# Performance work log

Measured on AMD Instinct MI355X. Metric: run time of the kernel, lower is better.

## Reference

```python
import jax, jax.numpy as jnp
import numpy as np

N_HEADS = 16
D_MODEL = 1024
HEAD_D = D_MODEL // N_HEADS


def setup_inputs() -> dict:
    key = jax.random.key(0)
    ks = jax.random.split(key, 8)
    B, S, D = 4, 2048, D_MODEL
    scale = 1.0 / np.sqrt(D)
    return {
        "query": jax.random.normal(ks[0], (B, S, D), jnp.float32),
        "key": jax.random.normal(ks[1], (B, S, D), jnp.float32),
        "value": jax.random.normal(ks[2], (B, S, D), jnp.float32),
        "mask": jax.random.randint(ks[3], (B, S, S), 0, 2, jnp.int32),
        "wq": jax.random.normal(ks[4], (D, D), jnp.float32) * scale,
        "wk": jax.random.normal(ks[5], (D, D), jnp.float32) * scale,
        "wv": jax.random.normal(ks[6], (D, D), jnp.float32) * scale,
        "w_out": jax.random.normal(ks[7], (D, D), jnp.float32) * scale,
    }


def reference(query, key, value, mask, wq, wk, wv, w_out):
    B, Sq, D = query.shape
    H, hd = N_HEADS, HEAD_D

    def split(x):  # (B,S,D) -> (B,H,S,hd)
        return x.reshape(B, -1, H, hd).transpose(0, 2, 1, 3)

    # torch Linear: y = x @ W.T (weights here stored as [out,in])
    Q = split(jnp.einsum('bsd,ed->bse', query, wq))
    K = split(jnp.einsum('bsd,ed->bse', key, wk))
    V = split(jnp.einsum('bsd,ed->bse', value, wv))

    scores = jnp.einsum('bhqd,bhkd->bhqk', Q, K) / np.sqrt(hd)
    scores = jnp.where(mask[:, None, :, :] == 1, jnp.float32(-1e9), scores)
    attn = jax.nn.softmax(scores, axis=-1)
    out = jnp.einsum('bhqk,bhkd->bhqd', attn, V)
    out = out.transpose(0, 2, 1, 3).reshape(B, Sq, D)
    return jnp.einsum('bsd,ed->bse', out, w_out)
```

## Files before the change

kernel.cpp:

```cpp
#include <hip/hip_runtime.h>
#include <hip/hip_bf16.h>


typedef __attribute__((ext_vector_type(8))) short short8;
typedef __attribute__((ext_vector_type(4))) float f32x4;
typedef __attribute__((ext_vector_type(4))) unsigned int u32x4;
typedef unsigned short u16;
typedef unsigned int u32;
typedef unsigned long long u64;

#define GLD16(gp, lp) __builtin_amdgcn_global_load_lds( \
    (const __attribute__((address_space(1))) void*)(gp), \
    (__attribute__((address_space(3))) void*)(lp), 16, 0, 0)

#if __has_builtin(__builtin_amdgcn_exp2f)
#define EXP2F(x) __builtin_amdgcn_exp2f(x)
#else
#define EXP2F(x) exp2f(x)
#endif

__device__ __forceinline__ u16 f2bf(float f) {
  u32 u = __builtin_bit_cast(u32, f);
  return (u16)((u + 0x7FFFu + ((u >> 16) & 1u)) >> 16);
}
__device__ __forceinline__ u32 swz64(u32 b)  { return b ^ (((b >> 7) & 3u) << 4); }
__device__ __forceinline__ u32 swz128(u32 b) { return b ^ (((b >> 7) & 7u) << 4); }

__global__ __launch_bounds__(256) void cvt_kernel(const float* __restrict__ in,
                                                  u16* __restrict__ out, float scale) {
  const size_t i = (size_t)blockIdx.x * 256 + threadIdx.x;
  f32x4 a = *(const f32x4*)(in + i * 8);
  f32x4 b = *(const f32x4*)(in + i * 8 + 4);
  u32x4 w;
  w.x = (u32)f2bf(a[0] * scale) | ((u32)f2bf(a[1] * scale) << 16);
  w.y = (u32)f2bf(a[2] * scale) | ((u32)f2bf(a[3] * scale) << 16);
  w.z = (u32)f2bf(b[0] * scale) | ((u32)f2bf(b[1] * scale) << 16);
  w.w = (u32)f2bf(b[2] * scale) | ((u32)f2bf(b[3] * scale) << 16);
  *(u32x4*)(out + i * 8) = w;
}

__global__ __launch_bounds__(256) void pack_mask_kernel(const int* __restrict__ m,
                                                        u64* __restrict__ out) {
  const size_t i = (size_t)blockIdx.x * 256 + threadIdx.x;
  u64 bal = __ballot(m[i] == 1);
  if ((threadIdx.x & 63) == 0) out[i >> 6] = bal;
}

template <int MODE>
__global__ __launch_bounds__(256)
void gemm_bt(const u16* __restrict__ A, const u16* __restrict__ W,
             void* __restrict__ outp, int K_) {
  __shared__ alignas(16) char sm[16384];
  const int tid = threadIdx.x, lane = tid & 63, wid = tid >> 6;
  const int g = lane >> 4, ln16 = lane & 15;
  const int wr = wid >> 1, wc = wid & 1;
  const int bm = blockIdx.y * 128, bn = blockIdx.x * 128;
  const int ldb = K_ * 2;

  u32 aoff[4], boff[4];
#pragma unroll
  for (int t = 0; t < 4; ++t) {
    aoff[t] = swz64(((u32)(wr * 64 + t * 16 + ln16) << 6) + ((u32)g << 4));
    boff[t] = 8192u + swz64(((u32)(wc * 64 + t * 16 + ln16) << 6) + ((u32)g << 4));
  }
  const char* ga[2]; const char* gw[2]; u32 doff[2];
#pragma unroll
  for (int i = 0; i < 2; ++i) {
    u32 lb = swz64((u32)(tid + i * 256) << 4);
    u32 row = lb >> 6, kbyte = lb & 63;
    ga[i] = (const char*)A + (size_t)(bm + row) * ldb + kbyte;
    gw[i] = (const char*)W + (size_t)(bn + row) * ldb + kbyte;
    doff[i] = (u32)(wid * 1024 + i * 4096);
  }
  f32x4 acc[4][4] = {};
  const int nk = K_ >> 5;
  for (int kt = 0; kt < nk; ++kt) {
    __syncthreads();
#pragma unroll
    for (int i = 0; i < 2; ++i) {
      GLD16(ga[i], sm + doff[i]);
      GLD16(gw[i], sm + 8192 + doff[i]);
      ga[i] += 64; gw[i] += 64;
    }
    __syncthreads();
    short8 aF[4], bF[4];
#pragma unroll
    for (int t = 0; t < 4; ++t) aF[t] = *(const short8*)(sm + aoff[t]);
#pragma unroll
    for (int t = 0; t < 4; ++t) bF[t] = *(const short8*)(sm + boff[t]);
#pragma unroll
    for (int mt = 0; mt < 4; ++mt)
#pragma unroll
      for (int nt = 0; nt < 4; ++nt)
        acc[mt][nt] = __builtin_amdgcn_mfma_f32_16x16x32_bf16(aF[mt], bF[nt], acc[mt][nt], 0, 0, 0);
  }
#pragma unroll
  for (int mt = 0; mt < 4; ++mt)
#pragma unroll
    for (int nt = 0; nt < 4; ++nt) {
      const f32x4 v = acc[mt][nt];
      const int row0 = bm + wr * 64 + mt * 16 + g * 4;
      const int col = bn + wc * 64 + nt * 16 + ln16;
      if (MODE == 2) {
        float* o = (float*)outp;
#pragma unroll
        for (int r = 0; r < 4; ++r) o[(size_t)(row0 + r) * 1024 + col] = v[r];
      } else if (MODE == 0) {
        u16* o = (u16*)outp;
        const int h = col >> 6, d = col & 63;
#pragma unroll
        for (int r = 0; r < 4; ++r) {
          const int row = row0 + r, b = row >> 11, s = row & 2047;
          o[((size_t)(b * 16 + h) * 2048 + s) * 64 + d] = f2bf(v[r]);
        }
      } else {
        u16* o = (u16*)outp;
        const int h = col >> 6, d = col & 63;
        const int b = row0 >> 11, s = row0 & 2047;
        u64 pv = (u64)f2bf(v[0]) | ((u64)f2bf(v[1]) << 16) |
                 ((u64)f2bf(v[2]) << 32) | ((u64)f2bf(v[3]) << 48);
        *(u64*)&o[((size_t)(b * 16 + h) * 64 + d) * 2048 + s] = pv;
      }
    }
}

__global__ __launch_bounds__(256)
void attn_kernel(const u16* __restrict__ Qh, const u16* __restrict__ Kh,
                 const u16* __restrict__ Vt, const u64* __restrict__ mp,
                 u16* __restrict__ AO) {
  __shared__ alignas(16) char sm[32768];
  const int tid = threadIdx.x, lane = tid & 63, wid = tid >> 6;
  const int g = lane >> 4, ln16 = lane & 15;
  char* Pl = sm + 16384 + wid * 4096;
  const int h = blockIdx.y, b = blockIdx.z;
  const int bh = b * 16 + h;
  const int q0 = blockIdx.x * 128 + wid * 32;
  const u16* Qb = Qh + (size_t)bh * 2048 * 64;
  const char* Kb = (const char*)Kh + (size_t)bh * 2048 * 128;
  const char* Vb = (const char*)Vt + (size_t)bh * 64 * 4096;

  short8 qf[2][2];
#pragma unroll
  for (int qs = 0; qs < 2; ++qs)
#pragma unroll
    for (int s = 0; s < 2; ++s)
      qf[qs][s] = *(const short8*)(Qb + (size_t)(q0 + qs * 16 + ln16) * 64 + s * 32 + g * 8);

  f32x4 acc[2][4] = {};
  float mx[2] = {-1e30f, -1e30f};
  float ls[2] = {0.f, 0.f};

  u32 srow[2], sbyt[2];
#pragma unroll
  for (int i = 0; i < 2; ++i) {
    u32 lb = swz128((u32)(tid + i * 256) << 4);
    srow[i] = lb >> 7; sbyt[i] = lb & 127;
  }
  const u64* mq = mp + ((size_t)b * 2048 + q0 + ln16) * 32;

  for (int kv = 0; kv < 2048; kv += 64) {
    __syncthreads();
#pragma unroll
    for (int i = 0; i < 2; ++i) {
      const u32 doff = (u32)(wid * 1024 + i * 4096);
      GLD16(Kb + (size_t)(kv + srow[i]) * 128 + sbyt[i], sm + doff);
      GLD16(Vb + (size_t)srow[i] * 4096 + (size_t)kv * 2 + sbyt[i], sm + 8192 + doff);
    }
    __syncthreads();

    u64 mw0 = mq[kv >> 6];
    u64 mw1 = mq[512 + (kv >> 6)];

    f32x4 sc[2][4] = {};
#pragma unroll
    for (int s = 0; s < 2; ++s)
#pragma unroll
      for (int kt = 0; kt < 4; ++kt) {
        short8 kf = *(const short8*)(sm + swz128(((u32)(kt * 16 + ln16) << 7) + s * 64 + g * 16));
        sc[0][kt] = __builtin_amdgcn_mfma_f32_16x16x32_bf16(kf, qf[0][s], sc[0][kt], 0, 0, 0);
        sc[1][kt] = __builtin_amdgcn_mfma_f32_16x16x32_bf16(kf, qf[1][s], sc[1][kt], 0, 0, 0);
      }

#pragma unroll
    for (int qs = 0; qs < 2; ++qs) {
      const u64 mw = qs ? mw1 : mw0;
      float tm = sc[qs][0][0];
#pragma unroll
      for (int kt = 0; kt < 4; ++kt)
#pragma unroll
        for (int r = 0; r < 4; ++r) tm = fmaxf(tm, sc[qs][kt][r]);
      tm = fmaxf(tm, __shfl_xor(tm, 16, 64));
      tm = fmaxf(tm, __shfl_xor(tm, 32, 64));
      const float mn = fmaxf(mx[qs], tm);
      const float corr = EXP2F(mx[qs] - mn);
      mx[qs] = mn;
      const u32 lo = (u32)mw, hi = (u32)(mw >> 32);
      float ps = 0.f;
#pragma unroll
      for (int kt = 0; kt < 4; ++kt) {
        const u32 nib = (((kt < 2) ? lo : hi) >> ((kt & 1) * 16 + g * 4)) & 0xFu;
        u64 pv = 0;
#pragma unroll
        for (int r = 0; r < 4; ++r) {
          float p = EXP2F(sc[qs][kt][r] - mn);
          if (nib & (1u << r)) p = 0.f;
          ps += p;
          pv |= (u64)f2bf(p) << (16 * r);
        }
        *(u64*)(Pl + swz128(((u32)(qs * 16 + ln16) << 7) + (u32)(kt * 32 + g * 8))) = pv;
      }
      ps += __shfl_xor(ps, 16, 64);
      ps += __shfl_xor(ps, 32, 64);
      ls[qs] = ls[qs] * corr + ps;
#pragma unroll
      for (int dt = 0; dt < 4; ++dt) acc[qs][dt] = acc[qs][dt] * corr;
    }
    asm volatile("" ::: "memory");

#pragma unroll
    for (int s = 0; s < 2; ++s) {
      short8 pf0 = *(const short8*)(Pl + swz128(((u32)ln16 << 7) + s * 64 + g * 16));
      short8 pf1 = *(const short8*)(Pl + swz128(((u32)(16 + ln16) << 7) + s * 64 + g * 16));
#pragma unroll
      for (int dt = 0; dt < 4; ++dt) {
        short8 vf = *(const short8*)(sm + 8192 + swz128(((u32)(dt * 16 + ln16) << 7) + s * 64 + g * 16));
        acc[0][dt] = __builtin_amdgcn_mfma_f32_16x16x32_bf16(vf, pf0, acc[0][dt], 0, 0, 0);
        acc[1][dt] = __builtin_amdgcn_mfma_f32_16x16x32_bf16(vf, pf1, acc[1][dt], 0, 0, 0);
      }
    }
    asm volatile("" ::: "memory");
  }

#pragma unroll
  for (int qs = 0; qs < 2; ++qs) {
    const float rl = 1.0f / ls[qs];
    const int q = q0 + qs * 16 + ln16;
#pragma unroll
    for (int dt = 0; dt < 4; ++dt) {
      const f32x4 v = acc[qs][dt];
      u64 pv = (u64)f2bf(v[0] * rl) | ((u64)f2bf(v[1] * rl) << 16) |
               ((u64)f2bf(v[2] * rl) << 32) | ((u64)f2bf(v[3] * rl) << 48);
      *(u64*)(AO + ((size_t)b * 2048 + q) * 1024 + h * 64 + dt * 16 + g * 4) = pv;
    }
  }
}

extern "C" void kernel_launch(void* const* d_in, const int* in_sizes, int n_in,
                              void* d_out, int out_size, void* d_ws, size_t ws_size,
                              hipStream_t stream) {
  const float* q   = (const float*)d_in[0];
  const float* k   = (const float*)d_in[1];
  const float* v   = (const float*)d_in[2];
  const int*   msk = (const int*)d_in[3];
  const float* wq  = (const float*)d_in[4];
  const float* wk  = (const float*)d_in[5];
  const float* wv  = (const float*)d_in[6];
  const float* wo  = (const float*)d_in[7];

  char* ws = (char*)d_ws;
  const size_t SZX = (size_t)8192 * 1024 * 2;
  const size_t SZW = (size_t)1024 * 1024 * 2;
  u16* qb  = (u16*)(ws + 0 * SZX);
  u16* kb  = (u16*)(ws + 1 * SZX);
  u16* vb  = (u16*)(ws + 2 * SZX);
  u16* wqb = (u16*)(ws + 3 * SZX + 0 * SZW);
  u16* wkb = (u16*)(ws + 3 * SZX + 1 * SZW);
  u16* wvb = (u16*)(ws + 3 * SZX + 2 * SZW);
  u16* wob = (u16*)(ws + 3 * SZX + 3 * SZW);
  u16* Qh  = (u16*)(ws + 3 * SZX + 4 * SZW);
  u16* Kh  = (u16*)(ws + 4 * SZX + 4 * SZW);
  u16* Vtp = (u16*)(ws + 5 * SZX + 4 * SZW);
  u16* AO  = qb;
  u64* mp  = (u64*)(ws + 6 * SZX + 4 * SZW);

  const float QSCALE = 0.18033688011112042f;

  cvt_kernel<<<4096, 256, 0, stream>>>(q, qb, 1.0f);
  cvt_kernel<<<4096, 256, 0, stream>>>(k, kb, 1.0f);
  cvt_kernel<<<4096, 256, 0, stream>>>(v, vb, 1.0f);
  cvt_kernel<<<512, 256, 0, stream>>>(wq, wqb, QSCALE);
  cvt_kernel<<<512, 256, 0, stream>>>(wk, wkb, 1.0f);
  cvt_kernel<<<512, 256, 0, stream>>>(wv, wvb, 1.0f);
  cvt_kernel<<<512, 256, 0, stream>>>(wo, wob, 1.0f);
  pack_mask_kernel<<<65536, 256, 0, stream>>>(msk, mp);

  gemm_bt<0><<<dim3(8, 64), 256, 0, stream>>>(qb, wqb, (void*)Qh, 1024);
  gemm_bt<0><<<dim3(8, 64), 256, 0, stream>>>(kb, wkb, (void*)Kh, 1024);
  gemm_bt<1><<<dim3(8, 64), 256, 0, stream>>>(vb, wvb, (void*)Vtp, 1024);

  attn_kernel<<<dim3(16, 16, 4), 256, 0, stream>>>(Qh, Kh, Vtp, mp, AO);

  gemm_bt<2><<<dim3(8, 64), 256, 0, stream>>>(AO, wob, d_out, 1024);
}
```

Baseline: 527.8 us.

## Double-buffer GEMM and attention loads, keep P in registers, use hardware bf16 convert

The GEMM now uses a 64-wide K tile with two LDS buffers, so the next tile's global-to-LDS load is issued before the current tile is computed. The attention kernel double-buffers K/V tiles the same way and prefetches mask words. It also keeps softmax probabilities in registers and feeds them to 16x16x16 MFMAs, which removes the LDS round trip for P. Manual bf16 rounding is replaced by v_cvt_pk_bf16_f32 throughout. The double buffering still has only one barrier per iteration, which could race between the async load into one buffer and reads of the previous one. The larger LDS use (64KB per GEMM block) may also reduce occupancy.

```diff
diff --git a/kernel.cpp b/kernel.cpp
--- a/kernel.cpp
+++ b/kernel.cpp
@@ -3,7 +3,9 @@
 
 
 typedef __attribute__((ext_vector_type(8))) short short8;
+typedef __attribute__((ext_vector_type(4))) short s16x4;
 typedef __attribute__((ext_vector_type(4))) float f32x4;
+typedef __attribute__((ext_vector_type(2))) unsigned int u32x2;
 typedef __attribute__((ext_vector_type(4))) unsigned int u32x4;
 typedef unsigned short u16;
 typedef unsigned int u32;
@@ -19,11 +21,30 @@
 #define EXP2F(x) exp2f(x)
 #endif
 
+#define MFMA32(a, b, c) __builtin_amdgcn_mfma_f32_16x16x32_bf16(a, b, c, 0, 0, 0)
+
+#if __has_builtin(__builtin_amdgcn_mfma_f32_16x16x16bf16_1k)
+__device__ __forceinline__ f32x4 mfma16(s16x4 a, s16x4 b, f32x4 c) {
+  return __builtin_amdgcn_mfma_f32_16x16x16bf16_1k(a, b, c, 0, 0, 0);
+}
+#else
+__device__ __forceinline__ f32x4 mfma16(s16x4 a, s16x4 b, f32x4 c) {
+  f32x4 d;
+  asm("v_mfma_f32_16x16x16_bf16 %0, %1, %2, %3"
+      : "=v"(d) : "v"(a), "v"(b), "0"(c));
+  return d;
+}
+#endif
+
 __device__ __forceinline__ u16 f2bf(float f) {
   u32 u = __builtin_bit_cast(u32, f);
   return (u16)((u + 0x7FFFu + ((u >> 16) & 1u)) >> 16);
 }
-__device__ __forceinline__ u32 swz64(u32 b)  { return b ^ (((b >> 7) & 3u) << 4); }
+__device__ __forceinline__ u32 cvtpk(float lo, float hi) {
+  u32 r;
+  asm("v_cvt_pk_bf16_f32 %0, %1, %2" : "=v"(r) : "v"(lo), "v"(hi));
+  return r;
+}
 __device__ __forceinline__ u32 swz128(u32 b) { return b ^ (((b >> 7) & 7u) << 4); }
 
 __global__ __launch_bounds__(256) void cvt_kernel(const float* __restrict__ in,
@@ -32,10 +53,10 @@
   f32x4 a = *(const f32x4*)(in + i * 8);
   f32x4 b = *(const f32x4*)(in + i * 8 + 4);
   u32x4 w;
-  w.x = (u32)f2bf(a[0] * scale) | ((u32)f2bf(a[1] * scale) << 16);
-  w.y = (u32)f2bf(a[2] * scale) | ((u32)f2bf(a[3] * scale) << 16);
-  w.z = (u32)f2bf(b[0] * scale) | ((u32)f2bf(b[1] * scale) << 16);
-  w.w = (u32)f2bf(b[2] * scale) | ((u32)f2bf(b[3] * scale) << 16);
+  w.x = cvtpk(a[0] * scale, a[1] * scale);
+  w.y = cvtpk(a[2] * scale, a[3] * scale);
+  w.z = cvtpk(b[0] * scale, b[1] * scale);
+  w.w = cvtpk(b[2] * scale, b[3] * scale);
   *(u32x4*)(out + i * 8) = w;
 }
 
@@ -50,49 +71,61 @@
 __global__ __launch_bounds__(256)
 void gemm_bt(const u16* __restrict__ A, const u16* __restrict__ W,
              void* __restrict__ outp, int K_) {
-  __shared__ alignas(16) char sm[16384];
+  __shared__ alignas(16) char sm[65536];
   const int tid = threadIdx.x, lane = tid & 63, wid = tid >> 6;
   const int g = lane >> 4, ln16 = lane & 15;
   const int wr = wid >> 1, wc = wid & 1;
   const int bm = blockIdx.y * 128, bn = blockIdx.x * 128;
   const int ldb = K_ * 2;
 
-  u32 aoff[4], boff[4];
-#pragma unroll
-  for (int t = 0; t < 4; ++t) {
-    aoff[t] = swz64(((u32)(wr * 64 + t * 16 + ln16) << 6) + ((u32)g << 4));
-    boff[t] = 8192u + swz64(((u32)(wc * 64 + t * 16 + ln16) << 6) + ((u32)g << 4));
-  }
-  const char* ga[2]; const char* gw[2]; u32 doff[2];
-#pragma unroll
-  for (int i = 0; i < 2; ++i) {
-    u32 lb = swz64((u32)(tid + i * 256) << 4);
-    u32 row = lb >> 6, kbyte = lb & 63;
+  u32 abase[2], bbase[2];
+#pragma unroll
+  for (int kk = 0; kk < 2; ++kk) {
+    const u32 sb = ((u32)(kk * 64 + g * 16)) ^ (((u32)ln16 & 7u) << 4);
+    abase[kk] = ((u32)(wr * 64 + ln16) << 7) + sb;
+    bbase[kk] = 16384u + ((u32)(wc * 64 + ln16) << 7) + sb;
+  }
+  const char* ga[4]; const char* gw[4];
+#pragma unroll
+  for (int i = 0; i < 4; ++i) {
+    u32 lb = swz128((u32)(tid + i * 256) << 4);
+    u32 row = lb >> 7, kbyte = lb & 127;
     ga[i] = (const char*)A + (size_t)(bm + row) * ldb + kbyte;
     gw[i] = (const char*)W + (size_t)(bn + row) * ldb + kbyte;
-    doff[i] = (u32)(wid * 1024 + i * 4096);
   }
   f32x4 acc[4][4] = {};
-  const int nk = K_ >> 5;
+  const int nk = K_ >> 6;
+  int cur = 0;
+
+#define G_STAGE(BUF)                                                  \
+  {                                                                   \
+    char* dst = sm + (BUF) * 32768 + wid * 1024;                      \
+    _Pragma("unroll") for (int i = 0; i < 4; ++i) {                   \
+      GLD16(ga[i], dst + i * 4096);                                   \
+      GLD16(gw[i], dst + 16384 + i * 4096);                           \
+      ga[i] += 128; gw[i] += 128;                                     \
+    }                                                                 \
+  }
+
+  G_STAGE(0);
   for (int kt = 0; kt < nk; ++kt) {
     __syncthreads();
-#pragma unroll
-    for (int i = 0; i < 2; ++i) {
-      GLD16(ga[i], sm + doff[i]);
-      GLD16(gw[i], sm + 8192 + doff[i]);
-      ga[i] += 64; gw[i] += 64;
-    }
-    __syncthreads();
-    short8 aF[4], bF[4];
-#pragma unroll
-    for (int t = 0; t < 4; ++t) aF[t] = *(const short8*)(sm + aoff[t]);
-#pragma unroll
-    for (int t = 0; t < 4; ++t) bF[t] = *(const short8*)(sm + boff[t]);
-#pragma unroll
-    for (int mt = 0; mt < 4; ++mt)
-#pragma unroll
-      for (int nt = 0; nt < 4; ++nt)
-        acc[mt][nt] = __builtin_amdgcn_mfma_f32_16x16x32_bf16(aF[mt], bF[nt], acc[mt][nt], 0, 0, 0);
+    if (kt + 1 < nk) G_STAGE(cur ^ 1);
+    const char* cb = sm + cur * 32768;
+#pragma unroll
+    for (int kk = 0; kk < 2; ++kk) {
+      short8 aF[4], bF[4];
+#pragma unroll
+      for (int t = 0; t < 4; ++t) aF[t] = *(const short8*)(cb + abase[kk] + t * 2048);
+#pragma unroll
+      for (int t = 0; t < 4; ++t) bF[t] = *(const short8*)(cb + bbase[kk] + t * 2048);
+#pragma unroll
+      for (int mt = 0; mt < 4; ++mt)
+#pragma unroll
+        for (int nt = 0; nt < 4; ++nt)
+          acc[mt][nt] = MFMA32(aF[mt], bF[nt], acc[mt][nt]);
+    }
+    cur ^= 1;
   }
 #pragma unroll
   for (int mt = 0; mt < 4; ++mt)
@@ -117,11 +150,11 @@
         u16* o = (u16*)outp;
         const int h = col >> 6, d = col & 63;
         const int b = row0 >> 11, s = row0 & 2047;
-        u64 pv = (u64)f2bf(v[0]) | ((u64)f2bf(v[1]) << 16) |
-                 ((u64)f2bf(v[2]) << 32) | ((u64)f2bf(v[3]) << 48);
-        *(u64*)&o[((size_t)(b * 16 + h) * 64 + d) * 2048 + s] = pv;
+        u32x2 pv; pv.x = cvtpk(v[0], v[1]); pv.y = cvtpk(v[2], v[3]);
+        *(u32x2*)&o[((size_t)(b * 16 + h) * 64 + d) * 2048 + s] = pv;
       }
     }
+#undef G_STAGE
 }
 
 __global__ __launch_bounds__(256)
@@ -131,9 +164,7 @@
   __shared__ alignas(16) char sm[32768];
   const int tid = threadIdx.x, lane = tid & 63, wid = tid >> 6;
   const int g = lane >> 4, ln16 = lane & 15;
-  char* Pl = sm + 16384 + wid * 4096;
-  const int h = blockIdx.y, b = blockIdx.z;
-  const int bh = b * 16 + h;
+  const int h = blockIdx.y, b = blockIdx.z, bh = b * 16 + h;
   const int q0 = blockIdx.x * 128 + wid * 32;
   const u16* Qb = Qh + (size_t)bh * 2048 * 64;
   const char* Kb = (const char*)Kh + (size_t)bh * 2048 * 128;
@@ -156,31 +187,49 @@
     u32 lb = swz128((u32)(tid + i * 256) << 4);
     srow[i] = lb >> 7; sbyt[i] = lb & 127;
   }
+  u32 kbase[2];
+#pragma unroll
+  for (int s = 0; s < 2; ++s)
+    kbase[s] = ((u32)ln16 << 7) + (((u32)(s * 64 + g * 16)) ^ (((u32)ln16 & 7u) << 4));
+  u32 vbyt[4];
+#pragma unroll
+  for (int kt = 0; kt < 4; ++kt)
+    vbyt[kt] = 8192u + ((u32)ln16 << 7) + (((u32)(kt * 32 + g * 8)) ^ (((u32)ln16 & 7u) << 4));
+
   const u64* mq = mp + ((size_t)b * 2048 + q0 + ln16) * 32;
 
-  for (int kv = 0; kv < 2048; kv += 64) {
+#define A_STAGE(KV, BUF)                                                        \
+  {                                                                             \
+    char* dst = sm + (BUF) * 16384 + wid * 1024;                                \
+    _Pragma("unroll") for (int i = 0; i < 2; ++i) {                             \
+      GLD16(Kb + (size_t)((KV) + srow[i]) * 128 + sbyt[i], dst + i * 4096);     \
+      GLD16(Vb + (size_t)srow[i] * 4096 + (size_t)(KV) * 2 + sbyt[i],           \
+            dst + 8192 + i * 4096);                                             \
+    }                                                                           \
+  }
+
+  int cur = 0;
+  A_STAGE(0, 0);
+  u64 mwc0 = mq[0], mwc1 = mq[512];
+
+  for (int kvt = 0; kvt < 32; ++kvt) {
     __syncthreads();
-#pragma unroll
-    for (int i = 0; i < 2; ++i) {
-      const u32 doff = (u32)(wid * 1024 + i * 4096);
-      GLD16(Kb + (size_t)(kv + srow[i]) * 128 + sbyt[i], sm + doff);
-      GLD16(Vb + (size_t)srow[i] * 4096 + (size_t)kv * 2 + sbyt[i], sm + 8192 + doff);
-    }
-    __syncthreads();
-
-    u64 mw0 = mq[kv >> 6];
-    u64 mw1 = mq[512 + (kv >> 6)];
+    if (kvt + 1 < 32) A_STAGE((kvt + 1) * 64, cur ^ 1);
+    const u64 mw0 = mwc0, mw1 = mwc1;
+    if (kvt + 1 < 32) { mwc0 = mq[kvt + 1]; mwc1 = mq[512 + kvt + 1]; }
+    const char* cb = sm + cur * 16384;
 
     f32x4 sc[2][4] = {};
 #pragma unroll
     for (int s = 0; s < 2; ++s)
 #pragma unroll
       for (int kt = 0; kt < 4; ++kt) {
-        short8 kf = *(const short8*)(sm + swz128(((u32)(kt * 16 + ln16) << 7) + s * 64 + g * 16));
-        sc[0][kt] = __builtin_amdgcn_mfma_f32_16x16x32_bf16(kf, qf[0][s], sc[0][kt], 0, 0, 0);
-        sc[1][kt] = __builtin_amdgcn_mfma_f32_16x16x32_bf16(kf, qf[1][s], sc[1][kt], 0, 0, 0);
+        short8 kfv = *(const short8*)(cb + kt * 2048 + kbase[s]);
+        sc[0][kt] = MFMA32(kfv, qf[0][s], sc[0][kt]);
+        sc[1][kt] = MFMA32(kfv, qf[1][s], sc[1][kt]);
       }
 
+    s16x4 pb[2][4];
 #pragma unroll
     for (int qs = 0; qs < 2; ++qs) {
       const u64 mw = qs ? mw1 : mw0;
@@ -199,15 +248,15 @@
 #pragma unroll
       for (int kt = 0; kt < 4; ++kt) {
         const u32 nib = (((kt < 2) ? lo : hi) >> ((kt & 1) * 16 + g * 4)) & 0xFu;
-        u64 pv = 0;
+        float p[4];
 #pragma unroll
         for (int r = 0; r < 4; ++r) {
-          float p = EXP2F(sc[qs][kt][r] - mn);
-          if (nib & (1u << r)) p = 0.f;
-          ps += p;
-          pv |= (u64)f2bf(p) << (16 * r);
+          p[r] = EXP2F(sc[qs][kt][r] - mn);
+          if (nib & (1u << r)) p[r] = 0.f;
+          ps += p[r];
         }
-        *(u64*)(Pl + swz128(((u32)(qs * 16 + ln16) << 7) + (u32)(kt * 32 + g * 8))) = pv;
+        u32x2 ww; ww.x = cvtpk(p[0], p[1]); ww.y = cvtpk(p[2], p[3]);
+        pb[qs][kt] = __builtin_bit_cast(s16x4, ww);
       }
       ps += __shfl_xor(ps, 16, 64);
       ps += __shfl_xor(ps, 32, 64);
@@ -215,21 +264,22 @@
 #pragma unroll
       for (int dt = 0; dt < 4; ++dt) acc[qs][dt] = acc[qs][dt] * corr;
     }
-    asm volatile("" ::: "memory");
-
-#pragma unroll
-    for (int s = 0; s < 2; ++s) {
-      short8 pf0 = *(const short8*)(Pl + swz128(((u32)ln16 << 7) + s * 64 + g * 16));
-      short8 pf1 = *(const short8*)(Pl + swz128(((u32)(16 + ln16) << 7) + s * 64 + g * 16));
+
+#pragma unroll
+    for (int kt = 0; kt < 4; ++kt) {
+      s16x4 vf[4];
+#pragma unroll
+      for (int dt = 0; dt < 4; ++dt)
+        vf[dt] = *(const s16x4*)(cb + vbyt[kt] + dt * 2048);
 #pragma unroll
       for (int dt = 0; dt < 4; ++dt) {
-        short8 vf = *(const short8*)(sm + 8192 + swz128(((u32)(dt * 16 + ln16) << 7) + s * 64 + g * 16));
-        acc[0][dt] = __builtin_amdgcn_mfma_f32_16x16x32_bf16(vf, pf0, acc[0][dt], 0, 0, 0);
-        acc[1][dt] = __builtin_amdgcn_mfma_f32_16x16x32_bf16(vf, pf1, acc[1][dt], 0, 0, 0);
+        acc[0][dt] = mfma16(vf[dt], pb[0][kt], acc[0][dt]);
+        acc[1][dt] = mfma16(vf[dt], pb[1][kt], acc[1][dt]);
       }
     }
-    asm volatile("" ::: "memory");
-  }
+    cur ^= 1;
+  }
+#undef A_STAGE
 
 #pragma unroll
   for (int qs = 0; qs < 2; ++qs) {
@@ -238,9 +288,8 @@
 #pragma unroll
     for (int dt = 0; dt < 4; ++dt) {
       const f32x4 v = acc[qs][dt];
-      u64 pv = (u64)f2bf(v[0] * rl) | ((u64)f2bf(v[1] * rl) << 16) |
-               ((u64)f2bf(v[2] * rl) << 32) | ((u64)f2bf(v[3] * rl) << 48);
-      *(u64*)(AO + ((size_t)b * 2048 + q) * 1024 + h * 64 + dt * 16 + g * 4) = pv;
+      u32x2 pv; pv.x = cvtpk(v[0] * rl, v[1] * rl); pv.y = cvtpk(v[2] * rl, v[3] * rl);
+      *(u32x2*)(AO + ((size_t)b * 2048 + q) * 1024 + h * 64 + dt * 16 + g * 4) = pv;
     }
   }
 }
```

After: 456.5 us. 1.16x faster.
